# Kernel optimization log

Measured on AMD Instinct MI355X. Metric: run time of the kernel, lower is better.

The kernel has to match this reference:

```python
import jax, jax.numpy as jnp
import numpy as np

HEADS = 8
DIM_HEAD = 64

def setup_inputs() -> dict:
    key = jax.random.key(0)
    k1, k2, k3 = jax.random.split(key, 3)
    B, L, D = 8, 4096, 512
    hidden = HEADS * DIM_HEAD  # 512
    x = jax.random.normal(k1, (B, L, D), dtype=jnp.float32)
    # Conv1d(kernel_size=1) weights, squeezed to 2D matrices
    Wqkv = jax.random.normal(k2, (3 * hidden, D), dtype=jnp.float32) * (1.0 / np.sqrt(D))
    Wout = jax.random.normal(k3, (D, hidden), dtype=jnp.float32) * (1.0 / np.sqrt(hidden))
    bout = jnp.zeros((D,), dtype=jnp.float32)
    return {"x": x, "Wqkv": Wqkv, "Wout": Wout, "bout": bout}

def reference(x, Wqkv, Wout, bout):
    B, L, D = x.shape
    H, C = HEADS, DIM_HEAD
    # pointwise conv == linear over channel dim: (b, 3*H*C, l)
    qkv = jnp.einsum('bld,od->bol', x, Wqkv)
    qkv = qkv.reshape(B, 3, H, C, L)  # channel split order: (qkv, heads, c)
    q, k, v = qkv[:, 0], qkv[:, 1], qkv[:, 2]  # each (b, h, c, l)
    k = jax.nn.softmax(k, axis=-1)   # softmax over sequence
    q = jax.nn.softmax(q, axis=-2)   # softmax over feature dim (q_norm=True)
    context = jnp.einsum('bhdn,bhen->bhde', k, v)   # (b,h,c,c)
    out = jnp.einsum('bhde,bhdn->bhen', context, q)  # (b,h,c,l)
    out = out.reshape(B, H * C, L)
    y = jnp.einsum('bcl,dc->bld', out, Wout) + bout  # to_out + permute back
    return y
```

## Files before the change

### kernel.cpp

```cpp
#include <hip/hip_runtime.h>

#define L 4096
#define D 512
#define NCH 16

typedef __bf16 bf16x8 __attribute__((ext_vector_type(8)));
typedef float  f32x4  __attribute__((ext_vector_type(4)));

__device__ __forceinline__ void load_lds16(const void* g, void* l) {
    __builtin_amdgcn_global_load_lds(
        (const __attribute__((address_space(1))) void*)g,
        (__attribute__((address_space(3))) void*)l, 16, 0, 0);
}

__device__ __forceinline__ void barrier_mem() {
    asm volatile("" ::: "memory");
    __builtin_amdgcn_s_barrier();
    asm volatile("" ::: "memory");
}

#define NX8  (8 * 4096 * 512 / 8)
#define NW18 (1536 * 512 / 8)
#define NW28 (512 * 512 / 8)
__global__ __launch_bounds__(256) void convert_all(const float* __restrict__ x,
                                                   const float* __restrict__ Wq,
                                                   const float* __restrict__ Wo,
                                                   __bf16* __restrict__ dst) {
    int i = blockIdx.x * 256 + threadIdx.x;
    if (i >= NX8 + NW18 + NW28) return;
    const float* s;
    if (i < NX8)             s = x  + (size_t)i * 8;
    else if (i < NX8 + NW18) s = Wq + (size_t)(i - NX8) * 8;
    else                     s = Wo + (size_t)(i - NX8 - NW18) * 8;
    float4 a = ((const float4*)s)[0], b = ((const float4*)s)[1];
    bf16x8 o = {(__bf16)a.x, (__bf16)a.y, (__bf16)a.z, (__bf16)a.w,
                (__bf16)b.x, (__bf16)b.y, (__bf16)b.z, (__bf16)b.w};
    *(bf16x8*)(dst + (size_t)i * 8) = o;
}

template <int M, int N, int K, typename CT>
__global__ __launch_bounds__(512, 2) void gemm_bf16_ws(
    const __bf16* __restrict__ A, size_t aStride,
    const __bf16* __restrict__ B, size_t bStride,
    CT* __restrict__ C, size_t cStride,
    const float* __restrict__ bias) {
    __shared__ __align__(16) __bf16 sB[2][256 * 64];
    __shared__ __align__(16) __bf16 sA[2][256 * 64];
    constexpr int NT = K / 64;
    const int b  = blockIdx.z;
    const int m0 = blockIdx.y * 256;
    const int n0 = blockIdx.x * 256;
    const int t    = threadIdx.x;
    const int wave = t >> 6, lane = t & 63;
    const int wm = (wave >> 2) * 128;
    const int wn = (wave & 3) * 64;
    const int fr = lane & 15, g = lane >> 4;
    const __bf16* Ab = A + (size_t)b * aStride + (size_t)m0 * K;
    const __bf16* Bb = B + (size_t)b * bStride + (size_t)n0 * K;
    CT* Cb = C + (size_t)b * cStride;

    const __bf16* pA_[4];
    const __bf16* pB_[4];
#pragma unroll
    for (int k = 0; k < 4; ++k) {
        const int gi = k * 512 + t, row = gi >> 3, cc = gi & 7;
        pA_[k] = Ab + (size_t)row * K + (cc ^ (row & 7)) * 8;
        pB_[k] = Bb + (size_t)row * K + (cc ^ (row & 7)) * 8;
    }
    const int lc0 = ((0 + g) ^ (fr & 7)) * 8;
    const int lc1 = ((4 + g) ^ (fr & 7)) * 8;

    f32x4 acc[8][4];
#pragma unroll
    for (int i = 0; i < 8; i++)
#pragma unroll
        for (int j = 0; j < 4; j++) acc[i][j] = (f32x4)(0.0f);

    auto stageT = [&](int kt, int pb) {
#pragma unroll
        for (int k = 0; k < 4; ++k) {
            load_lds16(pA_[k] + kt * 64, &sA[pb][(k * 512 + t) * 8]);
            load_lds16(pB_[k] + kt * 64, &sB[pb][(k * 512 + t) * 8]);
        }
    };

    stageT(0, 0);

#pragma unroll
    for (int kt = 0; kt < NT; ++kt) {
        const int p = kt & 1;
        asm volatile("s_waitcnt vmcnt(0)" ::: "memory");
        barrier_mem();
        if (kt + 1 < NT) stageT(kt + 1, p ^ 1);

        bf16x8 fB0[4], fB1[4], fA0[4], fA1[4], fA2[4], fA3[4];
#pragma unroll
        for (int j = 0; j < 4; ++j)
            fB0[j] = *(const bf16x8*)&sB[p][(wn + j * 16 + fr) * 64 + lc0];
#pragma unroll
        for (int i = 0; i < 4; ++i)
            fA0[i] = *(const bf16x8*)&sA[p][(wm + i * 16 + fr) * 64 + lc0];
#pragma unroll
        for (int i = 0; i < 4; ++i)
            fA1[i] = *(const bf16x8*)&sA[p][(wm + 64 + i * 16 + fr) * 64 + lc0];
        asm volatile("s_waitcnt lgkmcnt(4)" ::: "memory");
        __builtin_amdgcn_sched_barrier(0);
        __builtin_amdgcn_s_setprio(1);
#pragma unroll
        for (int i = 0; i < 4; ++i)
#pragma unroll
            for (int j = 0; j < 4; ++j)
                acc[i][j] = __builtin_amdgcn_mfma_f32_16x16x32_bf16(fA0[i], fB0[j], acc[i][j], 0, 0, 0);
        __builtin_amdgcn_s_setprio(0);
#pragma unroll
        for (int j = 0; j < 4; ++j)
            fB1[j] = *(const bf16x8*)&sB[p][(wn + j * 16 + fr) * 64 + lc1];
#pragma unroll
        for (int i = 0; i < 4; ++i)
            fA2[i] = *(const bf16x8*)&sA[p][(wm + i * 16 + fr) * 64 + lc1];
        asm volatile("s_waitcnt lgkmcnt(8)" ::: "memory");
        __builtin_amdgcn_sched_barrier(0);
        __builtin_amdgcn_s_setprio(1);
#pragma unroll
        for (int i = 0; i < 4; ++i)
#pragma unroll
            for (int j = 0; j < 4; ++j)
                acc[4 + i][j] = __builtin_amdgcn_mfma_f32_16x16x32_bf16(fA1[i], fB0[j], acc[4 + i][j], 0, 0, 0);
        __builtin_amdgcn_s_setprio(0);
#pragma unroll
        for (int i = 0; i < 4; ++i)
            fA3[i] = *(const bf16x8*)&sA[p][(wm + 64 + i * 16 + fr) * 64 + lc1];
        asm volatile("s_waitcnt lgkmcnt(4)" ::: "memory");
        __builtin_amdgcn_sched_barrier(0);
        __builtin_amdgcn_s_setprio(1);
#pragma unroll
        for (int i = 0; i < 4; ++i)
#pragma unroll
            for (int j = 0; j < 4; ++j)
                acc[i][j] = __builtin_amdgcn_mfma_f32_16x16x32_bf16(fA2[i], fB1[j], acc[i][j], 0, 0, 0);
        __builtin_amdgcn_s_setprio(0);
        asm volatile("s_waitcnt lgkmcnt(0)" ::: "memory");
        __builtin_amdgcn_sched_barrier(0);
        __builtin_amdgcn_s_setprio(1);
#pragma unroll
        for (int i = 0; i < 4; ++i)
#pragma unroll
            for (int j = 0; j < 4; ++j)
                acc[4 + i][j] = __builtin_amdgcn_mfma_f32_16x16x32_bf16(fA3[i], fB1[j], acc[4 + i][j], 0, 0, 0);
        __builtin_amdgcn_s_setprio(0);
    }

    const int rb = g * 4;
    float bv[4];
#pragma unroll
    for (int j = 0; j < 4; ++j) bv[j] = bias ? bias[n0 + wn + j * 16 + fr] : 0.0f;
#pragma unroll
    for (int i = 0; i < 8; ++i) {
#pragma unroll
        for (int r = 0; r < 4; ++r) {
            const int m = m0 + wm + i * 16 + rb + r;
            CT* rowp = Cb + (size_t)m * N + n0 + wn + fr;
#pragma unroll
            for (int j = 0; j < 4; ++j)
                rowp[j * 16] = (CT)(acc[i][j][r] + bv[j]);
        }
    }
}

#define SKS 264
__global__ __launch_bounds__(256) void context_local(const __bf16* __restrict__ qkv,
                                                     float* __restrict__ ctxp,
                                                     float* __restrict__ mstat,
                                                     float* __restrict__ sstat) {
    __shared__ __align__(16) __bf16 smem[2 * 64 * SKS];
    __bf16* sk = smem;
    __bf16* sv = smem + 64 * SKS;
    const int chunk = blockIdx.x;
    const int bh = blockIdx.y;
    const int b = bh >> 3, h = bh & 7;
    const __bf16* kbase = qkv + (size_t)b * 1536 * L + (size_t)(512 + h * 64) * L;
    const __bf16* vbase = qkv + (size_t)b * 1536 * L + (size_t)(1024 + h * 64) * L;
    const int t = threadIdx.x;

    {
        const int d = t >> 2, noff = (t & 3) * 64;
        const int n0 = chunk * 256;
        const __bf16* kp = kbase + (size_t)d * L + n0 + noff;
        const __bf16* vp = vbase + (size_t)d * L + n0 + noff;
        bf16x8 kk[8];
        float m = -1e30f;
#pragma unroll
        for (int c = 0; c < 8; c++) {
            kk[c] = *(const bf16x8*)(kp + c * 8);
            bf16x8 vv = *(const bf16x8*)(vp + c * 8);
            *(bf16x8*)&sv[d * SKS + noff + c * 8] = vv;
#pragma unroll
            for (int j = 0; j < 8; j++) m = fmaxf(m, (float)kk[c][j]);
        }
        m = fmaxf(m, __shfl_xor(m, 1, 64));
        m = fmaxf(m, __shfl_xor(m, 2, 64));
        float s = 0.f;
#pragma unroll
        for (int c = 0; c < 8; c++) {
            bf16x8 ek;
#pragma unroll
            for (int j = 0; j < 8; j++) {
                float e = __expf((float)kk[c][j] - m);
                s += e;
                ek[j] = (__bf16)e;
            }
            *(bf16x8*)&sk[d * SKS + noff + c * 8] = ek;
        }
        s += __shfl_xor(s, 1, 64);
        s += __shfl_xor(s, 2, 64);
        if ((t & 3) == 0) {
            mstat[((size_t)chunk * 64 + bh) * 64 + d] = m;
            sstat[((size_t)chunk * 64 + bh) * 64 + d] = s;
        }
    }
    __syncthreads();

    const int wave = t >> 6, lane = t & 63;
    const int fr = lane & 15, kq = (lane >> 4) * 8;
    f32x4 acc[4][4];
#pragma unroll
    for (int i = 0; i < 4; i++)
#pragma unroll
        for (int j = 0; j < 4; j++) acc[i][j] = (f32x4)(0.0f);
#pragma unroll
    for (int kh = 0; kh < 2; kh++) {
        const int koff = wave * 64 + kh * 32 + kq;
        bf16x8 af[4], bfr[4];
#pragma unroll
        for (int i = 0; i < 4; i++) {
            af[i]  = *(const bf16x8*)&sk[(i * 16 + fr) * SKS + koff];
            bfr[i] = *(const bf16x8*)&sv[(i * 16 + fr) * SKS + koff];
        }
#pragma unroll
        for (int i = 0; i < 4; i++)
#pragma unroll
            for (int j = 0; j < 4; j++)
                acc[i][j] = __builtin_amdgcn_mfma_f32_16x16x32_bf16(af[i], bfr[j], acc[i][j], 0, 0, 0);
    }
    __syncthreads();

    float* red = (float*)smem;
    const int col = lane & 15, rbase = (lane >> 4) * 4;
#pragma unroll
    for (int i = 0; i < 4; i++)
#pragma unroll
        for (int j = 0; j < 4; j++)
#pragma unroll
            for (int r = 0; r < 4; r++) {
                const int dd = i * 16 + rbase + r;
                const int ee = j * 16 + col;
                red[wave * 4096 + dd * 64 + ee] = acc[i][j][r];
            }
    __syncthreads();
    float* cp = ctxp + ((size_t)chunk * 64 + bh) * 4096;
#pragma unroll
    for (int gg = 0; gg < 4; gg++) {
        const int idx = t * 16 + gg * 4;
        f32x4 s = *(const f32x4*)&red[idx];
        s += *(const f32x4*)&red[4096 + idx];
        s += *(const f32x4*)&red[8192 + idx];
        s += *(const f32x4*)&red[12288 + idx];
        *(f32x4*)&cp[idx] = s;
    }
}

__global__ __launch_bounds__(256) void ctx_combine(const float* __restrict__ ctxp,
                                                   const float* __restrict__ mstat,
                                                   const float* __restrict__ sstat,
                                                   __bf16* __restrict__ ctxT) {
    const int bh = blockIdx.x >> 2, quarter = blockIdx.x & 3;
    const int t = threadIdx.x;
    const int flat = quarter * 1024 + t * 4;
    const int d = flat >> 6, e0 = flat & 63;
    float M = -1e30f;
#pragma unroll
    for (int ch = 0; ch < NCH; ch++)
        M = fmaxf(M, mstat[((size_t)ch * 64 + bh) * 64 + d]);
    float S = 0.f;
    float w[NCH];
#pragma unroll
    for (int ch = 0; ch < NCH; ch++) {
        w[ch] = __expf(mstat[((size_t)ch * 64 + bh) * 64 + d] - M);
        S += sstat[((size_t)ch * 64 + bh) * 64 + d] * w[ch];
    }
    const float inv = 1.0f / S;
    f32x4 s = (f32x4)(0.0f);
#pragma unroll
    for (int ch = 0; ch < NCH; ch++) {
        f32x4 v = *(const f32x4*)&ctxp[((size_t)ch * 64 + bh) * 4096 + flat];
        s += v * w[ch];
    }
    __bf16* o = ctxT + (size_t)bh * 4096;
#pragma unroll
    for (int j = 0; j < 4; j++) o[(e0 + j) * 64 + d] = (__bf16)(s[j] * inv);
}

#define SPS 66
__global__ __launch_bounds__(256) void pv_fused(__bf16* __restrict__ qkv,
                                                const __bf16* __restrict__ ctxT) {
    __shared__ __align__(16) __bf16 sp[256 * SPS];
    __shared__ __align__(16) __bf16 sctx[64 * SPS];
    __shared__ float sinv[256];
    const int tileN = blockIdx.x;
    const int bh = blockIdx.y;
    const int b = bh >> 3, h = bh & 7;
    const int t = threadIdx.x;
    const int n0 = tileN * 256;
    const __bf16* qbase = qkv + (size_t)b * 1536 * L + (size_t)(h * 64) * L;

    {
        const int e = t >> 2, c = t & 3;
        const bf16x8* src = (const bf16x8*)(ctxT + ((size_t)bh * 64 + e) * 64 + c * 16);
        *(bf16x8*)&sctx[e * SPS + c * 16] = src[0];
        *(bf16x8*)&sctx[e * SPS + c * 16 + 8] = src[1];
    }

    float m = -1e30f;
    float qv[64];
#pragma unroll
    for (int d = 0; d < 64; d++) {
        qv[d] = (float)qbase[(size_t)d * L + n0 + t];
        m = fmaxf(m, qv[d]);
    }
    float s = 0.f;
#pragma unroll
    for (int d0 = 0; d0 < 64; d0 += 8) {
        bf16x8 ek;
#pragma unroll
        for (int j = 0; j < 8; j++) {
            float e = __expf(qv[d0 + j] - m);
            s += e;
            ek[j] = (__bf16)e;
        }
        *(bf16x8*)&sp[t * SPS + d0] = ek;
    }
    sinv[t] = 1.0f / s;
    __syncthreads();

    const int wave = t >> 6, lane = t & 63;
    const int wm = wave * 64;
    const int fr = lane & 15, kq = (lane >> 4) * 8;
    f32x4 acc[4][4];
#pragma unroll
    for (int i = 0; i < 4; i++)
#pragma unroll
        for (int j = 0; j < 4; j++) acc[i][j] = (f32x4)(0.0f);
#pragma unroll
    for (int kh = 0; kh < 2; kh++) {
        bf16x8 af[4], bfr[4];
#pragma unroll
        for (int i = 0; i < 4; i++)
            af[i] = *(const bf16x8*)&sp[(wm + i * 16 + fr) * SPS + kh * 32 + kq];
#pragma unroll
        for (int j = 0; j < 4; j++)
            bfr[j] = *(const bf16x8*)&sctx[(j * 16 + fr) * SPS + kh * 32 + kq];
#pragma unroll
        for (int i = 0; i < 4; i++)
#pragma unroll
            for (int j = 0; j < 4; j++)
                acc[i][j] = __builtin_amdgcn_mfma_f32_16x16x32_bf16(af[i], bfr[j], acc[i][j], 0, 0, 0);
    }

    __bf16* ob = qkv + (size_t)b * 1536 * L + (size_t)512 * L;
    const int col = lane & 15, rbase = (lane >> 4) * 4;
#pragma unroll
    for (int i = 0; i < 4; i++) {
#pragma unroll
        for (int r = 0; r < 4; r++) {
            const int nl = wm + i * 16 + rbase + r;
            const float inv = sinv[nl];
            const size_t rowoff = (size_t)(n0 + nl) * 512 + h * 64;
#pragma unroll
            for (int j = 0; j < 4; j++)
                ob[rowoff + j * 16 + col] = (__bf16)(acc[i][j][r] * inv);
        }
    }
}

extern "C" void kernel_launch(void* const* d_in, const int* in_sizes, int n_in,
                              void* d_out, int out_size, void* d_ws, size_t ws_size,
                              hipStream_t stream) {
    const float* x    = (const float*)d_in[0];
    const float* Wqkv = (const float*)d_in[1];
    const float* Wout = (const float*)d_in[2];
    const float* bout = (const float*)d_in[3];
    float* y = (float*)d_out;

    __bf16* qkv   = (__bf16*)d_ws;
    float*  ctxp  = (float*)(qkv + (size_t)8 * 1536 * L);
    __bf16* xb    = (__bf16*)(ctxp + (size_t)NCH * 64 * 4096);
    __bf16* Wqb   = xb + (size_t)8 * 4096 * 512;
    __bf16* Wob   = Wqb + (size_t)1536 * 512;
    float*  mstat = (float*)(Wob + (size_t)512 * 512);
    float*  sstat = mstat + (size_t)NCH * 64 * 64;
    __bf16* ctxT  = (__bf16*)(sstat + (size_t)NCH * 64 * 64);

    const int convBlocks = (NX8 + NW18 + NW28 + 255) / 256;
    convert_all<<<dim3(convBlocks), 256, 0, stream>>>(x, Wqkv, Wout, xb);

    gemm_bf16_ws<1536, 4096, 512, __bf16><<<dim3(4096 / 256, 1536 / 256, 8), 512, 0, stream>>>(
        Wqb, 0, xb, (size_t)4096 * 512, qkv, (size_t)1536 * 4096, nullptr);

    context_local<<<dim3(NCH, 64), 256, 0, stream>>>(qkv, ctxp, mstat, sstat);
    ctx_combine<<<dim3(256), 256, 0, stream>>>(ctxp, mstat, sstat, ctxT);
    pv_fused<<<dim3(L / 256, 64), 256, 0, stream>>>(qkv, ctxT);

    const __bf16* outT = qkv + (size_t)512 * L;
    gemm_bf16_ws<4096, 512, 512, float><<<dim3(512 / 256, 4096 / 256, 8), 512, 0, stream>>>(
        outT, (size_t)1536 * L, Wob, 0, y, (size_t)4096 * 512, bout);
}
```

Measured before the change: 249.3 us.

## Fuse fp32-to-bf16 conversion into GEMM tile loads, drop separate convert pass

Removes the standalone convert kernel that cast x and both weight matrices to bf16 in workspace. The GEMM is now templated on input types. For fp32 operands it loads float4 pairs into registers two tiles ahead, converts them to bf16 and writes them into LDS, replacing the direct global-to-LDS loads. This saves a full read and write of the 64 MB activation tensor and one kernel launch. In exchange the GEMM reads twice the bytes per tile, holds more registers, and re-converts the weights in every block.

```diff
diff --git a/kernel.cpp b/kernel.cpp
--- a/kernel.cpp
+++ b/kernel.cpp
@@ -19,31 +19,14 @@
     asm volatile("" ::: "memory");
 }
 
-#define NX8  (8 * 4096 * 512 / 8)
-#define NW18 (1536 * 512 / 8)
-#define NW28 (512 * 512 / 8)
-__global__ __launch_bounds__(256) void convert_all(const float* __restrict__ x,
-                                                   const float* __restrict__ Wq,
-                                                   const float* __restrict__ Wo,
-                                                   __bf16* __restrict__ dst) {
-    int i = blockIdx.x * 256 + threadIdx.x;
-    if (i >= NX8 + NW18 + NW28) return;
-    const float* s;
-    if (i < NX8)             s = x  + (size_t)i * 8;
-    else if (i < NX8 + NW18) s = Wq + (size_t)(i - NX8) * 8;
-    else                     s = Wo + (size_t)(i - NX8 - NW18) * 8;
-    float4 a = ((const float4*)s)[0], b = ((const float4*)s)[1];
-    bf16x8 o = {(__bf16)a.x, (__bf16)a.y, (__bf16)a.z, (__bf16)a.w,
-                (__bf16)b.x, (__bf16)b.y, (__bf16)b.z, (__bf16)b.w};
-    *(bf16x8*)(dst + (size_t)i * 8) = o;
-}
-
-template <int M, int N, int K, typename CT>
-__global__ __launch_bounds__(512, 2) void gemm_bf16_ws(
-    const __bf16* __restrict__ A, size_t aStride,
-    const __bf16* __restrict__ B, size_t bStride,
+template <int M, int N, int K, typename AT, typename BT, typename CT>
+__global__ __launch_bounds__(512, 2) void gemm_ws2(
+    const AT* __restrict__ A, size_t aStride,
+    const BT* __restrict__ B, size_t bStride,
     CT* __restrict__ C, size_t cStride,
     const float* __restrict__ bias) {
+    constexpr bool AF = (sizeof(AT) == 4);
+    constexpr bool BF = (sizeof(BT) == 4);
     __shared__ __align__(16) __bf16 sB[2][256 * 64];
     __shared__ __align__(16) __bf16 sA[2][256 * 64];
     constexpr int NT = K / 64;
@@ -55,12 +38,12 @@
     const int wm = (wave >> 2) * 128;
     const int wn = (wave & 3) * 64;
     const int fr = lane & 15, g = lane >> 4;
-    const __bf16* Ab = A + (size_t)b * aStride + (size_t)m0 * K;
-    const __bf16* Bb = B + (size_t)b * bStride + (size_t)n0 * K;
+    const AT* Ab = A + (size_t)b * aStride + (size_t)m0 * K;
+    const BT* Bb = B + (size_t)b * bStride + (size_t)n0 * K;
     CT* Cb = C + (size_t)b * cStride;
 
-    const __bf16* pA_[4];
-    const __bf16* pB_[4];
+    const AT* pA_[4];
+    const BT* pB_[4];
 #pragma unroll
     for (int k = 0; k < 4; ++k) {
         const int gi = k * 512 + t, row = gi >> 3, cc = gi & 7;
@@ -76,22 +59,76 @@
 #pragma unroll
         for (int j = 0; j < 4; j++) acc[i][j] = (f32x4)(0.0f);
 
-    auto stageT = [&](int kt, int pb) {
-#pragma unroll
-        for (int k = 0; k < 4; ++k) {
-            load_lds16(pA_[k] + kt * 64, &sA[pb][(k * 512 + t) * 8]);
-            load_lds16(pB_[k] + kt * 64, &sB[pb][(k * 512 + t) * 8]);
-        }
-    };
-
-    stageT(0, 0);
+    float4 rA[4][2], rB[4][2];
+
+    auto loadA_f32 = [&](int kt) {
+        if constexpr (AF) {
+#pragma unroll
+            for (int k = 0; k < 4; ++k) {
+                rA[k][0] = *(const float4*)(pA_[k] + kt * 64);
+                rA[k][1] = *(const float4*)(pA_[k] + kt * 64 + 4);
+            }
+        }
+    };
+    auto loadB_f32 = [&](int kt) {
+        if constexpr (BF) {
+#pragma unroll
+            for (int k = 0; k < 4; ++k) {
+                rB[k][0] = *(const float4*)(pB_[k] + kt * 64);
+                rB[k][1] = *(const float4*)(pB_[k] + kt * 64 + 4);
+            }
+        }
+    };
+    auto loadA_lds = [&](int kt) {
+        if constexpr (!AF) {
+#pragma unroll
+            for (int k = 0; k < 4; ++k)
+                load_lds16(pA_[k] + kt * 64, &sA[kt & 1][(k * 512 + t) * 8]);
+        }
+    };
+    auto loadB_lds = [&](int kt) {
+        if constexpr (!BF) {
+#pragma unroll
+            for (int k = 0; k < 4; ++k)
+                load_lds16(pB_[k] + kt * 64, &sB[kt & 1][(k * 512 + t) * 8]);
+        }
+    };
+    auto cvt8 = [](float4 a, float4 c) -> bf16x8 {
+        return bf16x8{(__bf16)a.x, (__bf16)a.y, (__bf16)a.z, (__bf16)a.w,
+                      (__bf16)c.x, (__bf16)c.y, (__bf16)c.z, (__bf16)c.w};
+    };
+    auto writeA = [&](int pb) {
+        if constexpr (AF) {
+#pragma unroll
+            for (int k = 0; k < 4; ++k)
+                *(bf16x8*)&sA[pb][(k * 512 + t) * 8] = cvt8(rA[k][0], rA[k][1]);
+        }
+    };
+    auto writeB = [&](int pb) {
+        if constexpr (BF) {
+#pragma unroll
+            for (int k = 0; k < 4; ++k)
+                *(bf16x8*)&sB[pb][(k * 512 + t) * 8] = cvt8(rB[k][0], rB[k][1]);
+        }
+    };
+
+    loadA_f32(0); loadB_f32(0);
+    loadA_lds(0); loadB_lds(0);
+    if constexpr (AF || BF) {
+        asm volatile("s_waitcnt vmcnt(0)" ::: "memory");
+        writeA(0); writeB(0);
+        asm volatile("s_waitcnt lgkmcnt(0)" ::: "memory");
+        loadA_f32(1); loadB_f32(1);
+    }
 
 #pragma unroll
     for (int kt = 0; kt < NT; ++kt) {
         const int p = kt & 1;
         asm volatile("s_waitcnt vmcnt(0)" ::: "memory");
         barrier_mem();
-        if (kt + 1 < NT) stageT(kt + 1, p ^ 1);
+        if (kt + 1 < NT) { writeA(p ^ 1); writeB(p ^ 1); }
+        if (kt + 2 < NT) { loadA_f32(kt + 2); loadB_f32(kt + 2); }
+        if (kt + 1 < NT) { loadA_lds(kt + 1); loadB_lds(kt + 1); }
 
         bf16x8 fB0[4], fB1[4], fA0[4], fA1[4], fA2[4], fA3[4];
 #pragma unroll
@@ -393,24 +430,18 @@
 
     __bf16* qkv   = (__bf16*)d_ws;
     float*  ctxp  = (float*)(qkv + (size_t)8 * 1536 * L);
-    __bf16* xb    = (__bf16*)(ctxp + (size_t)NCH * 64 * 4096);
-    __bf16* Wqb   = xb + (size_t)8 * 4096 * 512;
-    __bf16* Wob   = Wqb + (size_t)1536 * 512;
-    float*  mstat = (float*)(Wob + (size_t)512 * 512);
+    float*  mstat = (float*)(ctxp + (size_t)NCH * 64 * 4096);
     float*  sstat = mstat + (size_t)NCH * 64 * 64;
     __bf16* ctxT  = (__bf16*)(sstat + (size_t)NCH * 64 * 64);
 
-    const int convBlocks = (NX8 + NW18 + NW28 + 255) / 256;
-    convert_all<<<dim3(convBlocks), 256, 0, stream>>>(x, Wqkv, Wout, xb);
-
-    gemm_bf16_ws<1536, 4096, 512, __bf16><<<dim3(4096 / 256, 1536 / 256, 8), 512, 0, stream>>>(
-        Wqb, 0, xb, (size_t)4096 * 512, qkv, (size_t)1536 * 4096, nullptr);
+    gemm_ws2<1536, 4096, 512, float, float, __bf16><<<dim3(4096 / 256, 1536 / 256, 8), 512, 0, stream>>>(
+        Wqkv, 0, x, (size_t)4096 * 512, qkv, (size_t)1536 * 4096, nullptr);
 
     context_local<<<dim3(NCH, 64), 256, 0, stream>>>(qkv, ctxp, mstat, sstat);
     ctx_combine<<<dim3(256), 256, 0, stream>>>(ctxp, mstat, sstat, ctxT);
     pv_fused<<<dim3(L / 256, 64), 256, 0, stream>>>(qkv, ctxT);
 
     const __bf16* outT = qkv + (size_t)512 * L;
-    gemm_bf16_ws<4096, 512, 512, float><<<dim3(512 / 256, 4096 / 256, 8), 512, 0, stream>>>(
-        outT, (size_t)1536 * L, Wob, 0, y, (size_t)4096 * 512, bout);
-}
+    gemm_ws2<4096, 512, 512, __bf16, float, float><<<dim3(512 / 256, 4096 / 256, 8), 512, 0, stream>>>(
+        outT, (size_t)1536 * L, Wout, 0, y, (size_t)4096 * 512, bout);
+}
```

Result: slower. 320.3 us (+28.5%).
